# Kernel tuning notes

Hardware: AMD Instinct MI355X
Metric: run time of the kernel (lower is better)

Reference implementation:

```python
import jax, jax.numpy as jnp
import numpy as np

N = 100000   # nodes
E = 1000000  # edges
D = 128      # in_dim == out_dim (residual enabled)
EPS = 1e-5   # BatchNorm1d default eps


def setup_inputs() -> dict:
    key = jax.random.key(0)
    k = jax.random.split(key, 5)
    feature = jax.random.normal(k[0], (N, D), dtype=jnp.float32)
    src = jax.random.randint(k[1], (E,), 0, N, dtype=jnp.int32)
    dst = jax.random.randint(k[2], (E,), 0, N, dtype=jnp.int32)
    # nn.Linear(in_dim, out_dim): W is [out, in]
    W = jax.random.normal(k[3], (D, D), dtype=jnp.float32) / np.sqrt(D).astype(np.float32)
    b = jnp.zeros((D,), dtype=jnp.float32)
    gamma = jnp.ones((D,), dtype=jnp.float32)
    beta = jnp.zeros((D,), dtype=jnp.float32)
    return {"feature": feature, "src": src, "dst": dst, "W": W, "b": b,
            "gamma": gamma, "beta": beta}


def reference(feature, src, dst, W, b, gamma, beta):
    # update_all(copy_src('h'), mean): gather src features, mean-reduce onto dst
    deg = jax.ops.segment_sum(jnp.ones((E,), dtype=feature.dtype), dst,
                              num_segments=N)                      # [N]
    agg = jax.ops.segment_sum(feature[src], dst, num_segments=N)   # [N, D]
    agg = agg / jnp.maximum(deg, 1.0)[:, None]  # zero in-degree -> 0 (DGL mean)
    # NodeApplyModule: linear
    h = agg @ W.T + b                                              # [N, D]
    # BatchNorm1d over node dimension (training-mode batch stats, biased var)
    mean = jnp.mean(h, axis=0)
    var = jnp.var(h, axis=0)
    h = (h - mean) * jax.lax.rsqrt(var + EPS) * gamma + beta
    # activation, residual; dropout p=0.0 -> identity
    h = jax.nn.relu(h)
    h = feature + h
    return h
```

## Files before the change

### kernel.cpp

```cpp
#include <hip/hip_runtime.h>

typedef unsigned short u16;
typedef unsigned int u32;

#define D_DIM 128
#define CHUNK 4096
#define NSTRIPE 64
#define LCN 12800

typedef __attribute__((ext_vector_type(8))) short bf16x8;
typedef __attribute__((ext_vector_type(4))) float f32x4;

__device__ __forceinline__ float bf2f(u16 h) {
    u32 u = ((u32)h) << 16;
    return __uint_as_float(u);
}
__device__ __forceinline__ u16 f2bf(float f) {
    u32 u = __float_as_uint(f);
    u32 r = (u >> 16) & 1u;
    u += 0x7fffu + r;
    return (u16)(u >> 16);
}
__device__ __forceinline__ float lo16(u32 u) { return bf2f((u16)(u & 0xffffu)); }
__device__ __forceinline__ float hi16(u32 u) { return bf2f((u16)(u >> 16)); }

__global__ void GCNLayer_76647986365164_kernel(
        int* p, int nwords, const u32* w, int* flag,
        const float* __restrict__ f, u16* __restrict__ fb,
        const void* __restrict__ W, u16* __restrict__ wpre,
        int total8, int zb) {
    const int tid = threadIdx.x;
    const int b = blockIdx.x;
    if (b < zb) {
        int i = b * 256 + tid;
        if (i < nwords) p[i] = 0;
        return;
    }
    __shared__ int cnt;
    if (tid == 0) cnt = 0;
    __syncthreads();
    {
        int c = 0;
        for (int j = 0; j < 4; ++j) {
            u32 x = w[tid * 4 + j];
            u32 e = (x >> 7) & 0xFFu;
            if (e >= 100u && e <= 140u) c++;
        }
        atomicAdd(&cnt, c);
    }
    __syncthreads();
    const int bf = (cnt >= 700) ? 1 : 0;
    if (b == zb && tid == 0) flag[0] = bf;

    if (b == gridDim.x - 1) {
        #pragma unroll
        for (int i = 0; i < 8; ++i) {
            int idx = i * 256 + tid;
            int frag = idx >> 6, dl = idx & 63;
            int ot = frag >> 2, kt = frag & 3;
            int dg = dl >> 4, dc = dl & 15;
            int row = ot * 16 + dc, col = kt * 32 + dg * 8;
            if (bf) {
                *(uint4*)(wpre + (size_t)idx * 8) =
                    *(const uint4*)((const u16*)W + row * 128 + col);
            } else {
                const float* Wf = (const float*)W;
                float4 x = *(const float4*)(Wf + row * 128 + col);
                float4 y = *(const float4*)(Wf + row * 128 + col + 4);
                float v[8] = {x.x, x.y, x.z, x.w, y.x, y.y, y.z, y.w};
                u16 h0[8], h1[8];
                #pragma unroll
                for (int j = 0; j < 8; ++j) {
                    h0[j] = f2bf(v[j]);
                    h1[j] = f2bf(v[j] - bf2f(h0[j]));
                }
                uint4 p0, p1;
                p0.x = (u32)h0[0] | ((u32)h0[1] << 16);
                p0.y = (u32)h0[2] | ((u32)h0[3] << 16);
                p0.z = (u32)h0[4] | ((u32)h0[5] << 16);
                p0.w = (u32)h0[6] | ((u32)h0[7] << 16);
                p1.x = (u32)h1[0] | ((u32)h1[1] << 16);
                p1.y = (u32)h1[2] | ((u32)h1[3] << 16);
                p1.z = (u32)h1[4] | ((u32)h1[5] << 16);
                p1.w = (u32)h1[6] | ((u32)h1[7] << 16);
                *(uint4*)(wpre + (size_t)idx * 8) = p0;
                *(uint4*)(wpre + 16384 + (size_t)idx * 8) = p1;
            }
        }
        return;
    }
    if (bf) return;
    int i = (b - zb) * 256 + tid;
    if (i >= total8) return;
    float4 a = ((const float4*)f)[i * 2];
    float4 bb = ((const float4*)f)[i * 2 + 1];
    uint4 o;
    o.x = (u32)f2bf(a.x) | ((u32)f2bf(a.y) << 16);
    o.y = (u32)f2bf(a.z) | ((u32)f2bf(a.w) << 16);
    o.z = (u32)f2bf(bb.x) | ((u32)f2bf(bb.y) << 16);
    o.w = (u32)f2bf(bb.z) | ((u32)f2bf(bb.w) << 16);
    ((uint4*)fb)[i] = o;
}

__global__ __launch_bounds__(256)
void k_hist(const int* __restrict__ dst, int* __restrict__ cnt,
            int E, int N, int nper, int ES, int P) {
    __shared__ int lc[LCN];
    const int tid = threadIdx.x;
    const int p = blockIdx.x % P;
    const int s = blockIdx.x / P;
    const int lo = p * nper;
    const int hi = min(lo + nper, N);
    const int cn = hi - lo;
    for (int t = tid; t < cn; t += 256) lc[t] = 0;
    __syncthreads();
    const int base = s * ES;
    const int end = min(base + ES, E);
    for (int i = base + tid * 4; i < end; i += 1024) {
        if (i + 3 < end) {
            int4 d4 = *(const int4*)(dst + i);
            if (d4.x >= lo && d4.x < hi) atomicAdd(&lc[d4.x - lo], 1);
            if (d4.y >= lo && d4.y < hi) atomicAdd(&lc[d4.y - lo], 1);
            if (d4.z >= lo && d4.z < hi) atomicAdd(&lc[d4.z - lo], 1);
            if (d4.w >= lo && d4.w < hi) atomicAdd(&lc[d4.w - lo], 1);
        } else {
            for (int k = i; k < end; ++k) {
                int d = dst[k];
                if (d >= lo && d < hi) atomicAdd(&lc[d - lo], 1);
            }
        }
    }
    __syncthreads();
    int* crow = cnt + (size_t)s * N + lo;
    for (int t = tid; t < cn; t += 256) crow[t] = lc[t];
}

__global__ void k_colscan(int* __restrict__ cnt, int* __restrict__ deg, int N) {
    int n = blockIdx.x * 256 + threadIdx.x;
    if (n >= N) return;
    int run = 0;
    #pragma unroll
    for (int s = 0; s < NSTRIPE; ++s) {
        int t = cnt[(size_t)s * N + n];
        cnt[(size_t)s * N + n] = run;
        run += t;
    }
    deg[n] = run;
}

__global__ void k_scan_local(const int* deg, int* offs, int* bsums, int n) {
    __shared__ int tsum[256];
    const int tid = threadIdx.x;
    const int base = blockIdx.x * CHUNK + tid * 16;
    int v[16];
    int run = 0;
    for (int j = 0; j < 16; ++j) {
        int idx = base + j;
        v[j] = (idx < n) ? deg[idx] : 0;
        run += v[j];
    }
    tsum[tid] = run;
    __syncthreads();
    for (int off = 1; off < 256; off <<= 1) {
        int val = tsum[tid];
        int add = (tid >= off) ? tsum[tid - off] : 0;
        __syncthreads();
        tsum[tid] = val + add;
        __syncthreads();
    }
    int acc = tsum[tid] - run;
    for (int j = 0; j < 16; ++j) {
        int idx = base + j;
        if (idx < n) offs[idx] = acc;
        acc += v[j];
    }
    if (tid == 255) bsums[blockIdx.x] = tsum[255];
}

__global__ void k_scan_add(int* offs, const int* bsums, int n, int nblk) {
    __shared__ int carry_s;
    const int tid = threadIdx.x;
    const int b = blockIdx.x;
    if (tid < 64) {
        int acc = 0;
        for (int k = tid; k < b; k += 64) acc += bsums[k];
        #pragma unroll
        for (int off = 1; off < 64; off <<= 1) acc += __shfl_xor(acc, off);
        if (tid == 0) {
            carry_s = acc;
            if (b == nblk - 1) offs[n] = acc + bsums[b];
        }
    }
    __syncthreads();
    const int carry = carry_s;
    const int base = b * CHUNK + tid * 16;
    for (int j = 0; j < 16; ++j) {
        int idx = base + j;
        if (idx < n) offs[idx] += carry;
    }
}

__global__ __launch_bounds__(256)
void k_scatter(const int* __restrict__ src, const int* __restrict__ dst,
               const int* __restrict__ bases, const int* __restrict__ offs,
               int* __restrict__ csr, int E, int N, int nper, int ES, int P) {
    __shared__ int lc[LCN];
    const int tid = threadIdx.x;
    const int p = blockIdx.x % P;
    const int s = blockIdx.x / P;
    const int lo = p * nper;
    const int hi = min(lo + nper, N);
    const int cn = hi - lo;
    const int* brow = bases + (size_t)s * N;
    for (int t = tid; t < cn; t += 256)
        lc[t] = offs[lo + t] + brow[lo + t];
    __syncthreads();
    const int base = s * ES;
    const int end = min(base + ES, E);
    for (int i = base + tid * 4; i < end; i += 1024) {
        if (i + 3 < end) {
            int4 d4 = *(const int4*)(dst + i);
            int4 s4 = *(const int4*)(src + i);
            if (d4.x >= lo && d4.x < hi) csr[atomicAdd(&lc[d4.x - lo], 1)] = s4.x;
            if (d4.y >= lo && d4.y < hi) csr[atomicAdd(&lc[d4.y - lo], 1)] = s4.y;
            if (d4.z >= lo && d4.z < hi) csr[atomicAdd(&lc[d4.z - lo], 1)] = s4.z;
            if (d4.w >= lo && d4.w < hi) csr[atomicAdd(&lc[d4.w - lo], 1)] = s4.w;
        } else {
            for (int k = i; k < end; ++k) {
                int d = dst[k];
                if (d >= lo && d < hi) csr[atomicAdd(&lc[d - lo], 1)] = src[k];
            }
        }
    }
}

__global__ __launch_bounds__(512, 8)
void k_agg_gemm(const void* feature, const u16* __restrict__ fcopy,
                const int* __restrict__ offs, const int* __restrict__ csr,
                const u16* __restrict__ wpre, const void* __restrict__ bias,
                u16* __restrict__ hout, float* __restrict__ parts,
                const int* __restrict__ flag, int n) {
    __shared__ u16 sBuf[128 * 136];
    const int tid = threadIdx.x;
    const int rb = blockIdx.x * 128;
    const int bf = flag[0];
    const u16* fbp = bf ? (const u16*)feature : fcopy;
    const uint4* fq = (const uint4*)fbp;

    {
        const int c = tid & 15;
        for (int pass = 0; pass < 4; ++pass) {
            const int nd = pass * 32 + (tid >> 4);
            const int node = rb + nd;
            float acc[8];
            #pragma unroll
            for (int t = 0; t < 8; ++t) acc[t] = 0.f;
            int degn = 0;
            if (node < n) {
                int s = offs[node], e = offs[node + 1];
                degn = e - s;
                for (int j = s; j < e; j += 4) {
                    int j1 = j + 1, j2 = j + 2, j3 = j + 3;
                    uint4 u0 = {0,0,0,0}, u1 = {0,0,0,0};
                    uint4 u2 = {0,0,0,0}, u3 = {0,0,0,0};
                    u0 = fq[(size_t)csr[j] * 16 + c];
                    if (j1 < e) u1 = fq[(size_t)csr[j1] * 16 + c];
                    if (j2 < e) u2 = fq[(size_t)csr[j2] * 16 + c];
                    if (j3 < e) u3 = fq[(size_t)csr[j3] * 16 + c];
                    #define ACC8(U) \
                        acc[0] += lo16(U.x); acc[1] += hi16(U.x); \
                        acc[2] += lo16(U.y); acc[3] += hi16(U.y); \
                        acc[4] += lo16(U.z); acc[5] += hi16(U.z); \
                        acc[6] += lo16(U.w); acc[7] += hi16(U.w);
                    ACC8(u0); ACC8(u1); ACC8(u2); ACC8(u3);
                    #undef ACC8
                }
            }
            float sc = 1.0f / (float)(degn > 1 ? degn : 1);
            uint4 o4;
            o4.x = (u32)f2bf(acc[0] * sc) | ((u32)f2bf(acc[1] * sc) << 16);
            o4.y = (u32)f2bf(acc[2] * sc) | ((u32)f2bf(acc[3] * sc) << 16);
            o4.z = (u32)f2bf(acc[4] * sc) | ((u32)f2bf(acc[5] * sc) << 16);
            o4.w = (u32)f2bf(acc[6] * sc) | ((u32)f2bf(acc[7] * sc) << 16);
            *(uint4*)(&sBuf[nd * 136 + c * 8]) = o4;
        }
    }
    __syncthreads();

    const int w = tid >> 6;
    const int lane = tid & 63;
    const int g = lane >> 4, cl = lane & 15;
    bf16x8 afr[4];
    #pragma unroll
    for (int kt = 0; kt < 4; ++kt)
        afr[kt] = *(const bf16x8*)(&sBuf[(w * 16 + cl) * 136 + g * 8 + kt * 32]);

    f32x4 acc[8];
    #pragma unroll
    for (int ot = 0; ot < 8; ++ot) acc[ot] = (f32x4){0.f, 0.f, 0.f, 0.f};

    const int npass = bf ? 1 : 2;
    for (int pass = 0; pass < npass; ++pass) {
        __syncthreads();
        const u16* wsrc = wpre + (size_t)pass * 16384;
        #pragma unroll
        for (int i = 0; i < 4; ++i) {
            int idx = i * 512 + tid;
            *(uint4*)(&sBuf[idx * 8]) = *(const uint4*)(wsrc + (size_t)idx * 8);
        }
        __syncthreads();
        #pragma unroll
        for (int ot = 0; ot < 8; ++ot) {
            #pragma unroll
            for (int kt = 0; kt < 4; ++kt) {
                bf16x8 bfr = *(const bf16x8*)(&sBuf[((ot * 4 + kt) * 64 + lane) * 8]);
                acc[ot] = __builtin_amdgcn_mfma_f32_16x16x32_bf16(
                    afr[kt], bfr, acc[ot], 0, 0, 0);
            }
        }
    }

    float* red = (float*)sBuf;
    __syncthreads();

    const int rowbase = rb + w * 16 + g * 4;
    #pragma unroll
    for (int ot = 0; ot < 8; ++ot) {
        const int o = ot * 16 + cl;
        float bv = bf ? bf2f(((const u16*)bias)[o]) : ((const float*)bias)[o];
        float s = 0.f, q = 0.f;
        float hv[4];
        #pragma unroll
        for (int r = 0; r < 4; ++r) {
            float h = acc[ot][r] + bv;
            hv[r] = h;
            if (rowbase + r < n) { s += h; q += h * h; }
        }
        #pragma unroll
        for (int r = 0; r < 4; ++r) {
            float hp = __shfl_xor(hv[r], 1);
            if (!(lane & 1)) {
                u32 pk = (u32)f2bf(hv[r]) | ((u32)f2bf(hp) << 16);
                *(u32*)(hout + (size_t)(rowbase + r) * D_DIM + o) = pk;
            }
        }
        s += __shfl_xor(s, 16); s += __shfl_xor(s, 32);
        q += __shfl_xor(q, 16); q += __shfl_xor(q, 32);
        if (g == 0) { red[w * 256 + o] = s; red[w * 256 + 128 + o] = q; }
    }
    __syncthreads();
    if (tid < 256) {
        float a = 0.f;
        #pragma unroll
        for (int ww = 0; ww < 8; ++ww) a += red[ww * 256 + tid];
        parts[(size_t)blockIdx.x * 256 + tid] = a;
    }
}

__global__ void k_redstats(const float* __restrict__ partials,
                           float* __restrict__ stats, int nb) {
    const int tid = threadIdx.x;
    float a0 = 0.f, a1 = 0.f, a2 = 0.f, a3 = 0.f;
    float a4 = 0.f, a5 = 0.f, a6 = 0.f, a7 = 0.f;
    for (int r0 = blockIdx.x * 8; r0 < nb; r0 += gridDim.x * 8) {
        if (r0 + 0 < nb) a0 += partials[(size_t)(r0 + 0) * 256 + tid];
        if (r0 + 1 < nb) a1 += partials[(size_t)(r0 + 1) * 256 + tid];
        if (r0 + 2 < nb) a2 += partials[(size_t)(r0 + 2) * 256 + tid];
        if (r0 + 3 < nb) a3 += partials[(size_t)(r0 + 3) * 256 + tid];
        if (r0 + 4 < nb) a4 += partials[(size_t)(r0 + 4) * 256 + tid];
        if (r0 + 5 < nb) a5 += partials[(size_t)(r0 + 5) * 256 + tid];
        if (r0 + 6 < nb) a6 += partials[(size_t)(r0 + 6) * 256 + tid];
        if (r0 + 7 < nb) a7 += partials[(size_t)(r0 + 7) * 256 + tid];
    }
    float s = ((a0 + a1) + (a2 + a3)) + ((a4 + a5) + (a6 + a7));
    atomicAdd(&stats[tid], s);
}

__global__ void k_apply(const u16* h, const void* feature, const float* stats,
                        const void* gamma, const void* beta, void* outp,
                        const int* flag, int total8, float invn) {
    __shared__ float ssc[128], ssh[128];
    int tid = threadIdx.x;
    int bf = flag[0];
    if (tid < 128) {
        float mean = stats[tid] * invn;
        float var = stats[128 + tid] * invn - mean * mean;
        var = fmaxf(var, 0.f);
        float inv = rsqrtf(var + 1e-5f);
        float g = bf ? bf2f(((const u16*)gamma)[tid]) : ((const float*)gamma)[tid];
        float bb = bf ? bf2f(((const u16*)beta)[tid]) : ((const float*)beta)[tid];
        float sc = inv * g;
        ssc[tid] = sc;
        ssh[tid] = bb - mean * sc;
    }
    __syncthreads();
    int i = blockIdx.x * 256 + tid;
    if (i >= total8) return;
    size_t base = (size_t)i * 8;
    int c0 = (int)(base & (D_DIM - 1));
    uint4 h4 = ((const uint4*)h)[i];
    u32 hw[4] = {h4.x, h4.y, h4.z, h4.w};
    float hv[8];
    for (int j = 0; j < 4; ++j) { hv[2*j] = lo16(hw[j]); hv[2*j+1] = hi16(hw[j]); }
    float fv[8];
    if (bf) {
        uint4 f4 = ((const uint4*)feature)[i];
        u32 fw[4] = {f4.x, f4.y, f4.z, f4.w};
        for (int j = 0; j < 4; ++j) { fv[2*j] = lo16(fw[j]); fv[2*j+1] = hi16(fw[j]); }
    } else {
        float4 fa = ((const float4*)feature)[i * 2];
        float4 fb = ((const float4*)feature)[i * 2 + 1];
        fv[0]=fa.x; fv[1]=fa.y; fv[2]=fa.z; fv[3]=fa.w;
        fv[4]=fb.x; fv[5]=fb.y; fv[6]=fb.z; fv[7]=fb.w;
    }
    float ov[8];
    for (int j = 0; j < 8; ++j)
        ov[j] = fmaxf(hv[j] * ssc[c0 + j] + ssh[c0 + j], 0.f) + fv[j];
    if (bf) {
        uint4 o4;
        u32 ow[4];
        for (int j = 0; j < 4; ++j)
            ow[j] = (u32)f2bf(ov[2*j]) | ((u32)f2bf(ov[2*j+1]) << 16);
        o4.x = ow[0]; o4.y = ow[1]; o4.z = ow[2]; o4.w = ow[3];
        ((uint4*)outp)[i] = o4;
    } else {
        float4 oa, ob;
        oa.x=ov[0]; oa.y=ov[1]; oa.z=ov[2]; oa.w=ov[3];
        ob.x=ov[4]; ob.y=ov[5]; ob.z=ov[6]; ob.w=ov[7];
        ((float4*)outp)[i * 2] = oa;
        ((float4*)outp)[i * 2 + 1] = ob;
    }
}

static inline size_t al256s(size_t x) { return (x + 255) & ~(size_t)255; }
static inline int gmax1(int x) { return x > 0 ? x : 1; }
static inline size_t smax(size_t a, size_t b) { return a > b ? a : b; }

extern "C" void kernel_launch(void* const* d_in, const int* in_sizes, int n_in,
                              void* d_out, int out_size, void* d_ws, size_t ws_size,
                              hipStream_t stream) {
    const void* feature = d_in[0];
    const int*  src     = (const int*)d_in[1];
    const int*  dst     = (const int*)d_in[2];
    const void* W       = d_in[3];
    const void* bias    = d_in[4];
    const void* gamma   = d_in[5];
    const void* beta    = d_in[6];

    const int N = in_sizes[0] / D_DIM;
    const int E = in_sizes[1];
    const int Npad = (N + 127) & ~127;
    const int nblk = (N + CHUNK - 1) / CHUNK;
    const int gb   = Npad / 128;

    int P = (N + LCN - 1) / LCN;  if (P < 8) P = 8;
    const int nper = (N + P - 1) / P;
    const int ES = (((E + NSTRIPE - 1) / NSTRIPE) + 3) & ~3;

    char* p = (char*)d_ws;
    size_t o = 0;
    int*   flag   = (int*)(p + o);      o += 256;
    int*   deg    = (int*)(p + o);      o += al256s((size_t)N * 4);
    float* stats  = (float*)(p + o);    o += 256 * 4;
    o = al256s(o);
    u16*   wpre   = (u16*)(p + o);      o += al256s(2 * 16384 * 2);
    int*   bsums  = (int*)(p + o);      o += al256s(((size_t)nblk + 8) * 4);
    int*   offs   = (int*)(p + o);      o += al256s(((size_t)N + 8) * 4);
    int*   csr    = (int*)(p + o);      o += al256s((size_t)E * 4);
    float* parts  = (float*)(p + o);    o += al256s((size_t)gb * 256 * 4);
    size_t hBytes   = (size_t)Npad * D_DIM * 2;
    size_t cntBytes = (size_t)NSTRIPE * N * 4;
    u16*   hbuf   = (u16*)(p + o);
    int*   cnt    = (int*)(p + o);      o += al256s(smax(hBytes, cntBytes));
    u16*   fbf    = (u16*)d_out;
    (void)ws_size; (void)n_in; (void)out_size;

    int total8 = N * D_DIM / 8;
    int zb = 1;
    int tb = gmax1((total8 + 255) / 256);
    int hblocks = NSTRIPE * P;

    GCNLayer_76647986365164_kernel<<<zb + tb + 1, 256, 0, stream>>>(
        (int*)stats, 256, (const u32*)feature, flag,
        (const float*)feature, fbf, W, wpre, total8, zb);
    k_hist<<<hblocks, 256, 0, stream>>>(dst, cnt, E, N, nper, ES, P);
    k_colscan<<<gmax1((N + 255) / 256), 256, 0, stream>>>(cnt, deg, N);
    k_scan_local<<<gmax1(nblk), 256, 0, stream>>>(deg, offs, bsums, N);
    k_scan_add<<<gmax1(nblk), 256, 0, stream>>>(offs, bsums, N, nblk);
    k_scatter<<<hblocks, 256, 0, stream>>>(src, dst, cnt, offs, csr,
                                           E, N, nper, ES, P);
    k_agg_gemm<<<gmax1(gb), 512, 0, stream>>>(
        feature, fbf, offs, csr, wpre, bias, hbuf, parts, flag, N);
    k_redstats<<<32, 256, 0, stream>>>(parts, stats, gb);
    k_apply<<<gmax1((total8 + 255) / 256), 256, 0, stream>>>(
        hbuf, feature, stats, gamma, beta, d_out, flag, total8, 1.0f / (float)N);
}
```

Baseline: 270.3 us.

## Fold scan carry-add into consumers and unroll gather loop to eight

Removes the separate k_scan_add kernel. k_scatter and k_agg_gemm now each compute block carries from bsums with a wave-level shuffle scan into LDS and add them when they read offs. The last local-scan block writes offs[n] locally, so the carry path supplies it. The aggregation gather loop is unrolled from 4 to 8 neighbors to put more loads in flight, and the launch-bounds occupancy hint is lowered from 8 to 6 to allow more registers. The carry scan assumes nblk ≤ 64 (N/4096 ≈ 25 here), and the extra registers may reduce occupancy.

```diff
diff --git a/kernel.cpp b/kernel.cpp
--- a/kernel.cpp
+++ b/kernel.cpp
@@ -23,6 +23,20 @@
 }
 __device__ __forceinline__ float lo16(u32 u) { return bf2f((u16)(u & 0xffffu)); }
 __device__ __forceinline__ float hi16(u32 u) { return bf2f((u16)(u >> 16)); }
+
+__device__ __forceinline__ void carry_scan(const int* __restrict__ bsums,
+                                           int* carryLds, int nblk, int tid) {
+    if (tid < 64) {
+        int v = (tid < nblk) ? bsums[tid] : 0;
+        int x = v;
+        #pragma unroll
+        for (int off = 1; off < 64; off <<= 1) {
+            int y = __shfl_up(x, off);
+            if (tid >= off) x += y;
+        }
+        carryLds[tid] = x - v;
+    }
+}
 
 __global__ void GCNLayer_76647986365164_kernel(
         int* p, int nwords, const u32* w, int* flag,
@@ -173,47 +187,32 @@
         int idx = base + j;
         if (idx < n) offs[idx] = acc;
         acc += v[j];
+        if (idx == n - 1) offs[n] = acc;
     }
     if (tid == 255) bsums[blockIdx.x] = tsum[255];
-}
-
-__global__ void k_scan_add(int* offs, const int* bsums, int n, int nblk) {
-    __shared__ int carry_s;
-    const int tid = threadIdx.x;
-    const int b = blockIdx.x;
-    if (tid < 64) {
-        int acc = 0;
-        for (int k = tid; k < b; k += 64) acc += bsums[k];
-        #pragma unroll
-        for (int off = 1; off < 64; off <<= 1) acc += __shfl_xor(acc, off);
-        if (tid == 0) {
-            carry_s = acc;
-            if (b == nblk - 1) offs[n] = acc + bsums[b];
-        }
-    }
-    __syncthreads();
-    const int carry = carry_s;
-    const int base = b * CHUNK + tid * 16;
-    for (int j = 0; j < 16; ++j) {
-        int idx = base + j;
-        if (idx < n) offs[idx] += carry;
-    }
 }
 
 __global__ __launch_bounds__(256)
 void k_scatter(const int* __restrict__ src, const int* __restrict__ dst,
                const int* __restrict__ bases, const int* __restrict__ offs,
-               int* __restrict__ csr, int E, int N, int nper, int ES, int P) {
+               const int* __restrict__ bsums, int* __restrict__ csr,
+               int E, int N, int nper, int ES, int P, int nblk) {
     __shared__ int lc[LCN];
+    __shared__ int carryLds[64];
     const int tid = threadIdx.x;
     const int p = blockIdx.x % P;
     const int s = blockIdx.x / P;
     const int lo = p * nper;
     const int hi = min(lo + nper, N);
     const int cn = hi - lo;
+    carry_scan(bsums, carryLds, nblk, tid);
+    __syncthreads();
     const int* brow = bases + (size_t)s * N;
-    for (int t = tid; t < cn; t += 256)
-        lc[t] = offs[lo + t] + brow[lo + t];
+    const int nblkm1 = nblk - 1;
+    for (int t = tid; t < cn; t += 256) {
+        int idx = lo + t;
+        lc[t] = offs[idx] + carryLds[min(idx >> 12, nblkm1)] + brow[idx];
+    }
     __syncthreads();
     const int base = s * ES;
     const int end = min(base + ES, E);
@@ -234,18 +233,24 @@
     }
 }
 
-__global__ __launch_bounds__(512, 8)
+__global__ __launch_bounds__(512, 6)
 void k_agg_gemm(const void* feature, const u16* __restrict__ fcopy,
                 const int* __restrict__ offs, const int* __restrict__ csr,
+                const int* __restrict__ bsums,
                 const u16* __restrict__ wpre, const void* __restrict__ bias,
                 u16* __restrict__ hout, float* __restrict__ parts,
-                const int* __restrict__ flag, int n) {
+                const int* __restrict__ flag, int n, int nblk) {
     __shared__ u16 sBuf[128 * 136];
+    __shared__ int carryLds[64];
     const int tid = threadIdx.x;
     const int rb = blockIdx.x * 128;
     const int bf = flag[0];
     const u16* fbp = bf ? (const u16*)feature : fcopy;
     const uint4* fq = (const uint4*)fbp;
+    const int nblkm1 = nblk - 1;
+
+    carry_scan(bsums, carryLds, nblk, tid);
+    __syncthreads();
 
     {
         const int c = tid & 15;
@@ -257,22 +262,28 @@
             for (int t = 0; t < 8; ++t) acc[t] = 0.f;
             int degn = 0;
             if (node < n) {
-                int s = offs[node], e = offs[node + 1];
+                int s = offs[node] + carryLds[min(node >> 12, nblkm1)];
+                int e = offs[node + 1] + carryLds[min((node + 1) >> 12, nblkm1)];
                 degn = e - s;
-                for (int j = s; j < e; j += 4) {
-                    int j1 = j + 1, j2 = j + 2, j3 = j + 3;
-                    uint4 u0 = {0,0,0,0}, u1 = {0,0,0,0};
-                    uint4 u2 = {0,0,0,0}, u3 = {0,0,0,0};
+                for (int j = s; j < e; j += 8) {
+                    uint4 u0 = {0,0,0,0}, u1 = {0,0,0,0}, u2 = {0,0,0,0},
+                          u3 = {0,0,0,0}, u4 = {0,0,0,0}, u5 = {0,0,0,0},
+                          u6 = {0,0,0,0}, u7 = {0,0,0,0};
                     u0 = fq[(size_t)csr[j] * 16 + c];
-                    if (j1 < e) u1 = fq[(size_t)csr[j1] * 16 + c];
-                    if (j2 < e) u2 = fq[(size_t)csr[j2] * 16 + c];
-                    if (j3 < e) u3 = fq[(size_t)csr[j3] * 16 + c];
+                    if (j + 1 < e) u1 = fq[(size_t)csr[j + 1] * 16 + c];
+                    if (j + 2 < e) u2 = fq[(size_t)csr[j + 2] * 16 + c];
+                    if (j + 3 < e) u3 = fq[(size_t)csr[j + 3] * 16 + c];
+                    if (j + 4 < e) u4 = fq[(size_t)csr[j + 4] * 16 + c];
+                    if (j + 5 < e) u5 = fq[(size_t)csr[j + 5] * 16 + c];
+                    if (j + 6 < e) u6 = fq[(size_t)csr[j + 6] * 16 + c];
+                    if (j + 7 < e) u7 = fq[(size_t)csr[j + 7] * 16 + c];
                     #define ACC8(U) \
                         acc[0] += lo16(U.x); acc[1] += hi16(U.x); \
                         acc[2] += lo16(U.y); acc[3] += hi16(U.y); \
                         acc[4] += lo16(U.z); acc[5] += hi16(U.z); \
                         acc[6] += lo16(U.w); acc[7] += hi16(U.w);
                     ACC8(u0); ACC8(u1); ACC8(u2); ACC8(u3);
+                    ACC8(u4); ACC8(u5); ACC8(u6); ACC8(u7);
                     #undef ACC8
                 }
             }
@@ -486,11 +497,10 @@
     k_hist<<<hblocks, 256, 0, stream>>>(dst, cnt, E, N, nper, ES, P);
     k_colscan<<<gmax1((N + 255) / 256), 256, 0, stream>>>(cnt, deg, N);
     k_scan_local<<<gmax1(nblk), 256, 0, stream>>>(deg, offs, bsums, N);
-    k_scan_add<<<gmax1(nblk), 256, 0, stream>>>(offs, bsums, N, nblk);
-    k_scatter<<<hblocks, 256, 0, stream>>>(src, dst, cnt, offs, csr,
-                                           E, N, nper, ES, P);
+    k_scatter<<<hblocks, 256, 0, stream>>>(src, dst, cnt, offs, bsums, csr,
+                                           E, N, nper, ES, P, nblk);
     k_agg_gemm<<<gmax1(gb), 512, 0, stream>>>(
-        feature, fbf, offs, csr, wpre, bias, hbuf, parts, flag, N);
+        feature, fbf, offs, csr, bsums, wpre, bias, hbuf, parts, flag, N, nblk);
     k_redstats<<<32, 256, 0, stream>>>(parts, stats, gb);
     k_apply<<<gmax1((total8 + 255) / 256), 256, 0, stream>>>(
         hbuf, feature, stats, gamma, beta, d_out, flag, total8, 1.0f / (float)N);
```

Measured after the change: 293.9 us. 8.7% more time.
